# Optimization experiments

Hardware: AMD Instinct MI355X
Metric: run time of the kernel (lower is better)

Reference implementation:

```python
import jax, jax.numpy as jnp
import numpy as np

K = 7  # kernel_size
D = 2  # dilation


def window_start(idx, L, K, D):
    """NATTEN neighborhood window start (clamped at borders, dilation-group aware)."""
    nh = K // 2
    if D <= 1:
        return jnp.maximum(idx - nh, 0) + jnp.where(idx + nh >= L, L - idx - nh - 1, 0)
    ni = idx - nh * D
    imodd = idx % D
    a = (L // D) * D
    b = L - a
    right = jnp.where(imodd < b, L - b + imodd - 2 * nh * D, a + imodd - K * D)
    return jnp.where(ni < 0, imodd, jnp.where(idx + nh * D >= L, right, ni))


def setup_inputs() -> dict:
    key = jax.random.key(0)
    ks = jax.random.split(key, 7)
    B, Cin, H, W, Cout = 2, 128, 112, 112, 64
    x = jax.random.normal(ks[0], (B, Cin, H, W), dtype=jnp.float32)
    Wq = jax.random.normal(ks[1], (Cout, Cin), dtype=jnp.float32) * 0.02
    Wk = jax.random.normal(ks[2], (Cout, Cin), dtype=jnp.float32) * 0.02
    Wv = jax.random.normal(ks[3], (Cout, Cin), dtype=jnp.float32) * 0.02
    bq = jax.random.normal(ks[4], (Cout,), dtype=jnp.float32) * 0.02
    bk = jax.random.normal(ks[5], (Cout,), dtype=jnp.float32) * 0.02
    bv = jax.random.normal(ks[6], (Cout,), dtype=jnp.float32) * 0.02
    return {"x": x, "Wq": Wq, "bq": bq, "Wk": Wk, "bk": bk, "Wv": Wv, "bv": bv}


def reference(x, Wq, bq, Wk, bk, Wv, bv):
    B, Cin, H, W = x.shape
    # 1x1 conv projections -> channels-last [B, H, W, C]
    q = jnp.einsum('bchw,oc->bhwo', x, Wq) + bq
    k = jnp.einsum('bchw,oc->bhwo', x, Wk) + bk
    v = jnp.einsum('bchw,oc->bhwo', x, Wv) + bv
    C = q.shape[-1]
    scale = jnp.asarray(C, q.dtype) ** -0.5  # NATTEN default scale (heads=1, head_dim=C)

    offs = jnp.arange(K) * D
    ih = window_start(jnp.arange(H), H, K, D)[:, None] + offs  # [H, K]
    iw = window_start(jnp.arange(W), W, K, D)[:, None] + offs  # [W, K]
    # gather neighborhoods -> [B, H, W, K, K, C]
    idx_h = ih[:, None, :, None]  # [H,1,K,1]
    idx_w = iw[None, :, None, :]  # [1,W,1,K]
    kw = k[:, idx_h, idx_w, :]
    vw = v[:, idx_h, idx_w, :]

    scores = jnp.einsum('bhwc,bhwijc->bhwij', q * scale, kw)  # [B,H,W,K,K]
    attn = jax.nn.softmax(scores.reshape(B, H, W, K * K), axis=-1)
    out = jnp.einsum('bhwn,bhwnc->bhwc', attn, vw.reshape(B, H, W, K * K, C))
    return out.transpose(0, 3, 1, 2)  # [B, C, H, W]
```

## Files before the change

kernel.cpp:

```cpp
#include <hip/hip_runtime.h>
#include <hip/hip_bf16.h>

#define HWSZ 12544
#define WDIM 112
#define CIN  128
#define NPIX 25088
#define VTROW 6272
#define VTOFF (2 * (size_t)NPIX * 64)

typedef __attribute__((ext_vector_type(8))) short          short8;
typedef __attribute__((ext_vector_type(4))) float          float4v;
typedef __attribute__((ext_vector_type(4))) unsigned short ushort4v;

__device__ __forceinline__ int window_start7x2(int idx, int L) {
    int ni = idx - 6;
    int imodd = idx & 1;
    int a = (L >> 1) << 1;
    int bb = L - a;
    int right = (imodd < bb) ? (L - bb + imodd - 12) : (a + imodd - 14);
    if (ni < 0) return imodd;
    if (idx + 6 >= L) return right;
    return ni;
}

__device__ __forceinline__ unsigned short f2bf(float f) {
    __hip_bfloat16 h = __float2bfloat16(f);
    return *(unsigned short*)&h;
}

__global__ __launch_bounds__(256) void proj_mfma(
    const float* __restrict__ x,
    const float* __restrict__ Wq, const float* __restrict__ bq,
    const float* __restrict__ Wk, const float* __restrict__ bk,
    const float* __restrict__ Wv, const float* __restrict__ bv,
    unsigned short* __restrict__ qbuf)
{
    __shared__ __align__(16) unsigned short wsb[3][64][136];
    __shared__ __align__(16) unsigned short trans[64 * 80];

    const int t = threadIdx.x, lane = t & 63, wv = t >> 6, quad = lane >> 4;
    const int col = lane & 15;

    const int tile = blockIdx.x;
    const int pix0 = tile * 64;
    const int b    = tile / 196;
    const int hw0  = pix0 - b * HWSZ;
    const float* xb = x + (size_t)b * CIN * HWSZ;

    #pragma unroll
    for (int m = 0; m < 3; ++m) {
        const float* Wm = (m == 0) ? Wq : (m == 1) ? Wk : Wv;
        #pragma unroll
        for (int i = 0; i < 8; ++i) {
            int u = t + 256 * i;
            int o = u >> 5, cq = (u & 31) * 4;
            float4 w4 = *(const float4*)&Wm[o * 128 + cq];
            ushort4v s4 = { f2bf(w4.x), f2bf(w4.y), f2bf(w4.z), f2bf(w4.w) };
            *(ushort4v*)&wsb[m][o][cq] = s4;
        }
    }

    const int hwpx = hw0 + wv * 16 + col;
    short8 af[4];
    #pragma unroll
    for (int kc = 0; kc < 4; ++kc) {
        #pragma unroll
        for (int j = 0; j < 8; ++j) {
            int c = kc * 32 + quad * 8 + j;
            af[kc][j] = (short)f2bf(xb[(size_t)c * HWSZ + hwpx]);
        }
    }
    __syncthreads();

    float4v acc[3][4];
    #pragma unroll
    for (int m = 0; m < 3; ++m)
        #pragma unroll
        for (int nt = 0; nt < 4; ++nt)
            acc[m][nt] = (float4v){0, 0, 0, 0};

    #pragma unroll
    for (int kc = 0; kc < 4; ++kc) {
        #pragma unroll
        for (int m = 0; m < 3; ++m) {
            #pragma unroll
            for (int nt = 0; nt < 4; ++nt) {
                short8 bfv = *(const short8*)&wsb[m][nt * 16 + col][kc * 32 + quad * 8];
                acc[m][nt] = __builtin_amdgcn_mfma_f32_16x16x32_bf16(af[kc], bfv, acc[m][nt], 0, 0, 0);
            }
        }
    }
    __syncthreads();

    #pragma unroll
    for (int m = 0; m < 2; ++m) {
        const float scale = (m == 0) ? 0.125f : 1.0f;
        const float* bm = (m == 0) ? bq : bk;
        #pragma unroll
        for (int nt = 0; nt < 4; ++nt) {
            float bias = bm[nt * 16 + col];
            #pragma unroll
            for (int r = 0; r < 4; ++r) {
                int px = wv * 16 + quad * 4 + r;
                trans[px * 80 + nt * 16 + col] = f2bf((acc[m][nt][r] + bias) * scale);
            }
        }
        __syncthreads();
        unsigned short* outm = qbuf + (size_t)m * NPIX * 64;
        const int tpx = t >> 2, chunk = t & 3;
        const unsigned short* src = &trans[tpx * 80 + chunk * 16];
        unsigned short* dst = outm + (size_t)(pix0 + tpx) * 64 + chunk * 16;
        *(short8*)(dst)     = *(const short8*)(src);
        *(short8*)(dst + 8) = *(const short8*)(src + 8);
        __syncthreads();
    }

    {
        #pragma unroll
        for (int nt = 0; nt < 4; ++nt) {
            int ch = nt * 16 + col;
            float bias = bv[ch];
            #pragma unroll
            for (int r = 0; r < 4; ++r) {
                int px = wv * 16 + quad * 4 + r;
                trans[ch * 80 + (px & 1) * 40 + (px >> 1)] = f2bf(acc[2][nt][r] + bias);
            }
        }
        __syncthreads();
        unsigned short* vt = qbuf + VTOFF;
        const int ch = t >> 2, parity = (t >> 1) & 1, half = t & 1;
        const unsigned short* src = &trans[ch * 80 + parity * 40 + half * 16];
        unsigned short* dst = vt + (size_t)((b * 2 + parity) * 64 + ch) * VTROW
                            + (hw0 >> 1) + half * 16;
        *(short8*)(dst)     = *(const short8*)(src);
        *(short8*)(dst + 8) = *(const short8*)(src + 8);
    }
}

__global__ __launch_bounds__(128) void attn_mfma(
    const unsigned short* __restrict__ qkv, float* __restrict__ out)
{
    __shared__ __align__(16) unsigned short ps[2][16 * 232];
    __shared__ __align__(16) float lds_out[64 * 36];

    const int lane = threadIdx.x & 63, g = threadIdx.x >> 6;
    const int quad = lane >> 4, col = lane & 15;

    const int bx   = blockIdx.x;
    const int xcd  = bx & 7;
    const int idx  = bx >> 3;
    const int h    = xcd * 14 + (idx >> 3);
    const int b    = (idx >> 2) & 1;
    const int sub  = idx & 3;
    const int pb   = (sub < 3) ? sub * 16 : 40;

    const int hs  = window_start7x2(h, WDIM);
    const int ws0 = window_start7x2(2 * pb + g, WDIM);
    const int cb0 = (ws0 >> 1) & ~7;
    const int pixbase = b * HWSZ;

    const unsigned short* qg = qkv;
    const unsigned short* kg = qkv + (size_t)NPIX * 64;
    const unsigned short* vt = qkv + VTOFF + (size_t)(b * 2 + g) * 64 * VTROW;

    const int qpix = pixbase + h * WDIM + 2 * (pb + col) + g;
    short8 af0 = *(const short8*)(qg + (size_t)qpix * 64 + quad * 8);
    short8 af1 = *(const short8*)(qg + (size_t)qpix * 64 + 32 + quad * 8);

    int cbr[4];
    #pragma unroll
    for (int r = 0; r < 4; ++r)
        cbr[r] = (window_start7x2(2 * (pb + quad * 4 + r) + g, WDIM) >> 1) - cb0;

    int rowoff[7];
    #pragma unroll
    for (int kc = 0; kc < 7; ++kc) {
        int u8 = kc * 32 + quad * 8;
        rowoff[kc] = (hs + 2 * (u8 >> 5)) * 56 + cb0 + (u8 & 31);
    }
    short8 vpre[4][4];
    #pragma unroll
    for (int kc = 0; kc < 4; ++kc)
        #pragma unroll
        for (int nt = 0; nt < 4; ++nt)
            vpre[kc][nt] = *(const short8*)
                (vt + (size_t)(nt * 16 + col) * VTROW + rowoff[kc]);

    float4v S[14];
    #pragma unroll
    for (int nt = 0; nt < 14; ++nt) {
        int u = nt * 16 + col;
        int i = u >> 5, c = u & 31;
        int wcol = cb0 + c;
        int kw = 2 * wcol + g; kw = (kw > 111) ? 111 : kw;
        int kp = pixbase + (hs + 2 * i) * WDIM + kw;
        float4v a = {0, 0, 0, 0};
        __builtin_amdgcn_s_setprio(1);
        a = __builtin_amdgcn_mfma_f32_16x16x32_bf16(
                af0, *(const short8*)(kg + (size_t)kp * 64 + quad * 8), a, 0, 0, 0);
        a = __builtin_amdgcn_mfma_f32_16x16x32_bf16(
                af1, *(const short8*)(kg + (size_t)kp * 64 + 32 + quad * 8), a, 0, 0, 0);
        __builtin_amdgcn_s_setprio(0);
        bool colok = (wcol <= 55);
        #pragma unroll
        for (int r = 0; r < 4; ++r) {
            bool valid = colok && ((unsigned)(c - cbr[r]) < 7u);
            S[nt][r] = valid ? a[r] : -1e30f;
        }
    }

    #pragma unroll
    for (int r = 0; r < 4; ++r) {
        float sum = 0.0f;
        #pragma unroll
        for (int nt = 0; nt < 14; ++nt) {
            float e = __expf(S[nt][r]);
            S[nt][r] = e;
            sum += e;
        }
        #pragma unroll
        for (int msk = 1; msk < 16; msk <<= 1)
            sum += __shfl_xor(sum, msk, 64);
        float rinv = 1.0f / sum;
        int row = quad * 4 + r;
        #pragma unroll
        for (int nt = 0; nt < 14; ++nt)
            ps[g][row * 232 + nt * 16 + col] = f2bf(S[nt][r] * rinv);
    }

    float4v O[4] = {{0,0,0,0},{0,0,0,0},{0,0,0,0},{0,0,0,0}};
    #pragma unroll
    for (int kc = 0; kc < 4; ++kc) {
        short8 pa = *(const short8*)&ps[g][col * 232 + kc * 32 + quad * 8];
        __builtin_amdgcn_s_setprio(1);
        #pragma unroll
        for (int nt = 0; nt < 4; ++nt)
            O[nt] = __builtin_amdgcn_mfma_f32_16x16x32_bf16(pa, vpre[kc][nt], O[nt], 0, 0, 0);
        __builtin_amdgcn_s_setprio(0);
    }
    #pragma unroll
    for (int kc = 4; kc < 7; ++kc) {
        short8 pa = *(const short8*)&ps[g][col * 232 + kc * 32 + quad * 8];
        #pragma unroll
        for (int nt = 0; nt < 4; ++nt) {
            short8 vb = *(const short8*)(vt + (size_t)(nt * 16 + col) * VTROW + rowoff[kc]);
            __builtin_amdgcn_s_setprio(1);
            O[nt] = __builtin_amdgcn_mfma_f32_16x16x32_bf16(pa, vb, O[nt], 0, 0, 0);
            __builtin_amdgcn_s_setprio(0);
        }
    }

    #pragma unroll
    for (int nt = 0; nt < 4; ++nt) {
        int ch = nt * 16 + col;
        #pragma unroll
        for (int r = 0; r < 4; ++r)
            lds_out[ch * 36 + 2 * (quad * 4 + r) + g] = O[nt][r];
    }
    __syncthreads();

    {
        const int ch = threadIdx.x >> 1, half = threadIdx.x & 1;
        float* ob = out + (size_t)(b * 64 + ch) * HWSZ + h * WDIM + 2 * pb + half * 16;
        const float* src = &lds_out[ch * 36 + half * 16];
        #pragma unroll
        for (int j = 0; j < 4; ++j)
            *(float4*)(ob + j * 4) = *(const float4*)(src + j * 4);
    }
}

extern "C" void kernel_launch(void* const* d_in, const int* in_sizes, int n_in,
                              void* d_out, int out_size, void* d_ws, size_t ws_size,
                              hipStream_t stream) {
    const float* x  = (const float*)d_in[0];
    const float* Wq = (const float*)d_in[1];
    const float* bq = (const float*)d_in[2];
    const float* Wk = (const float*)d_in[3];
    const float* bk = (const float*)d_in[4];
    const float* Wv = (const float*)d_in[5];
    const float* bv = (const float*)d_in[6];
    float* out = (float*)d_out;

    unsigned short* qkv = (unsigned short*)d_ws;

    proj_mfma<<<dim3(392), dim3(256), 0, stream>>>(x, Wq, bq, Wk, bk, Wv, bv, qkv);
    attn_mfma<<<dim3(896), dim3(128), 0, stream>>>(qkv, out);
}
```

Measured before the change: 95.56 us.

## Split attention work across four waves per block with deferred softmax normalization

Doubles the attention block from two to four waves. Each pair of waves now splits the 14 key tiles for QK^T and the 64 output channels for PV. Partial softmax sums are exchanged through shared memory with an extra barrier, and normalization is deferred to the output write. This roughly halves per-wave register use and serial MFMA work, and all V tiles are now prefetched up front, which should improve latency hiding and occupancy. The cost is an added block-wide sync and more waves competing per CU.

After: 97.50 us. 2.0% more time.

```diff
diff --git a/kernel.cpp b/kernel.cpp
--- a/kernel.cpp
+++ b/kernel.cpp
@@ -137,13 +137,17 @@
     }
 }
 
-__global__ __launch_bounds__(128) void attn_mfma(
+__global__ __launch_bounds__(256) void attn_mfma(
     const unsigned short* __restrict__ qkv, float* __restrict__ out)
 {
     __shared__ __align__(16) unsigned short ps[2][16 * 232];
+    __shared__ __align__(16) float sums_lds[2][2][16];
     __shared__ __align__(16) float lds_out[64 * 36];
 
-    const int lane = threadIdx.x & 63, g = threadIdx.x >> 6;
+    const int tid  = threadIdx.x;
+    const int lane = tid & 63, wid = tid >> 6;
+    const int g    = wid & 1;
+    const int vh   = wid >> 1;
     const int quad = lane >> 4, col = lane & 15;
 
     const int bx   = blockIdx.x;
@@ -178,18 +182,19 @@
         int u8 = kc * 32 + quad * 8;
         rowoff[kc] = (hs + 2 * (u8 >> 5)) * 56 + cb0 + (u8 & 31);
     }
-    short8 vpre[4][4];
-    #pragma unroll
-    for (int kc = 0; kc < 4; ++kc)
-        #pragma unroll
-        for (int nt = 0; nt < 4; ++nt)
-            vpre[kc][nt] = *(const short8*)
-                (vt + (size_t)(nt * 16 + col) * VTROW + rowoff[kc]);
-
-    float4v S[14];
-    #pragma unroll
-    for (int nt = 0; nt < 14; ++nt) {
-        int u = nt * 16 + col;
+    short8 vpre[7][2];
+    #pragma unroll
+    for (int kc = 0; kc < 7; ++kc)
+        #pragma unroll
+        for (int ntl = 0; ntl < 2; ++ntl)
+            vpre[kc][ntl] = *(const short8*)
+                (vt + (size_t)(vh * 32 + ntl * 16 + col) * VTROW + rowoff[kc]);
+
+    float4v S[7];
+    #pragma unroll
+    for (int ntl = 0; ntl < 7; ++ntl) {
+        int ntg = vh * 7 + ntl;
+        int u = ntg * 16 + col;
         int i = u >> 5, c = u & 31;
         int wcol = cb0 + c;
         int kw = 2 * wcol + g; kw = (kw > 111) ? 111 : kw;
@@ -205,67 +210,69 @@
         #pragma unroll
         for (int r = 0; r < 4; ++r) {
             bool valid = colok && ((unsigned)(c - cbr[r]) < 7u);
-            S[nt][r] = valid ? a[r] : -1e30f;
-        }
-    }
-
+            S[ntl][r] = valid ? a[r] : -1e30f;
+        }
+    }
+
+    float psum[4];
     #pragma unroll
     for (int r = 0; r < 4; ++r) {
         float sum = 0.0f;
         #pragma unroll
-        for (int nt = 0; nt < 14; ++nt) {
-            float e = __expf(S[nt][r]);
-            S[nt][r] = e;
+        for (int ntl = 0; ntl < 7; ++ntl) {
+            float e = __expf(S[ntl][r]);
+            S[ntl][r] = e;
             sum += e;
         }
         #pragma unroll
         for (int msk = 1; msk < 16; msk <<= 1)
             sum += __shfl_xor(sum, msk, 64);
-        float rinv = 1.0f / sum;
+        psum[r] = sum;
         int row = quad * 4 + r;
         #pragma unroll
-        for (int nt = 0; nt < 14; ++nt)
-            ps[g][row * 232 + nt * 16 + col] = f2bf(S[nt][r] * rinv);
-    }
-
-    float4v O[4] = {{0,0,0,0},{0,0,0,0},{0,0,0,0},{0,0,0,0}};
-    #pragma unroll
-    for (int kc = 0; kc < 4; ++kc) {
+        for (int ntl = 0; ntl < 7; ++ntl)
+            ps[g][row * 232 + (vh * 7 + ntl) * 16 + col] = f2bf(S[ntl][r]);
+    }
+    if (col == 0) {
+        #pragma unroll
+        for (int r = 0; r < 4; ++r)
+            sums_lds[g][vh][quad * 4 + r] = psum[r];
+    }
+    __syncthreads();
+
+    float rinv[4];
+    #pragma unroll
+    for (int r = 0; r < 4; ++r) {
+        int row = quad * 4 + r;
+        rinv[r] = 1.0f / (sums_lds[g][0][row] + sums_lds[g][1][row]);
+    }
+
+    float4v O[2] = {{0,0,0,0},{0,0,0,0}};
+    #pragma unroll
+    for (int kc = 0; kc < 7; ++kc) {
         short8 pa = *(const short8*)&ps[g][col * 232 + kc * 32 + quad * 8];
         __builtin_amdgcn_s_setprio(1);
         #pragma unroll
-        for (int nt = 0; nt < 4; ++nt)
-            O[nt] = __builtin_amdgcn_mfma_f32_16x16x32_bf16(pa, vpre[kc][nt], O[nt], 0, 0, 0);
+        for (int ntl = 0; ntl < 2; ++ntl)
+            O[ntl] = __builtin_amdgcn_mfma_f32_16x16x32_bf16(pa, vpre[kc][ntl], O[ntl], 0, 0, 0);
         __builtin_amdgcn_s_setprio(0);
     }
-    #pragma unroll
-    for (int kc = 4; kc < 7; ++kc) {
-        short8 pa = *(const short8*)&ps[g][col * 232 + kc * 32 + quad * 8];
-        #pragma unroll
-        for (int nt = 0; nt < 4; ++nt) {
-            short8 vb = *(const short8*)(vt + (size_t)(nt * 16 + col) * VTROW + rowoff[kc]);
-            __builtin_amdgcn_s_setprio(1);
-            O[nt] = __builtin_amdgcn_mfma_f32_16x16x32_bf16(pa, vb, O[nt], 0, 0, 0);
-            __builtin_amdgcn_s_setprio(0);
-        }
-    }
-
-    #pragma unroll
-    for (int nt = 0; nt < 4; ++nt) {
-        int ch = nt * 16 + col;
+
+    #pragma unroll
+    for (int ntl = 0; ntl < 2; ++ntl) {
+        int ch = vh * 32 + ntl * 16 + col;
         #pragma unroll
         for (int r = 0; r < 4; ++r)
-            lds_out[ch * 36 + 2 * (quad * 4 + r) + g] = O[nt][r];
+            lds_out[ch * 36 + 2 * (quad * 4 + r) + g] = O[ntl][r] * rinv[r];
     }
     __syncthreads();
 
     {
-        const int ch = threadIdx.x >> 1, half = threadIdx.x & 1;
-        float* ob = out + (size_t)(b * 64 + ch) * HWSZ + h * WDIM + 2 * pb + half * 16;
-        const float* src = &lds_out[ch * 36 + half * 16];
-        #pragma unroll
-        for (int j = 0; j < 4; ++j)
-            *(float4*)(ob + j * 4) = *(const float4*)(src + j * 4);
+        const int ch = tid >> 2, q4 = tid & 3;
+        float* ob = out + (size_t)(b * 64 + ch) * HWSZ + h * WDIM + 2 * pb + q4 * 8;
+        const float* src = &lds_out[ch * 36 + q4 * 8];
+        *(float4*)(ob)     = *(const float4*)(src);
+        *(float4*)(ob + 4) = *(const float4*)(src + 4);
     }
 }
 
@@ -284,5 +291,5 @@
     unsigned short* qkv = (unsigned short*)d_ws;
 
     proj_mfma<<<dim3(392), dim3(256), 0, stream>>>(x, Wq, bq, Wk, bk, Wv, bv, qkv);
-    attn_mfma<<<dim3(896), dim3(128), 0, stream>>>(qkv, out);
-}
+    attn_mfma<<<dim3(896), dim3(256), 0, stream>>>(qkv, out);
+}
```
